# Performance work log

Measured on AMD Instinct MI355X. Metric: run time of the kernel, lower is better.

## Reference

```python
import jax, jax.numpy as jnp
import numpy as np

NUM_HEADS = 12
QUERY_SCALE = 0.125  # hard-coded 1/sqrt(64) in the original module


def setup_inputs() -> dict:
    key = jax.random.key(0)
    ks = jax.random.split(key, 5)
    S, B, H = 1024, 8, 768
    return {
        "hidden_states": jax.random.normal(ks[0], (S, B, H), dtype=jnp.float32),
        "in_proj_weight": jax.random.normal(ks[1], (3 * H, H), dtype=jnp.float32) * 0.02,
        "in_proj_bias": jax.random.normal(ks[2], (3 * H,), dtype=jnp.float32) * 0.02,
        "out_proj_weight": jax.random.normal(ks[3], (H, H), dtype=jnp.float32) * 0.02,
        "out_proj_bias": jax.random.normal(ks[4], (H,), dtype=jnp.float32) * 0.02,
    }


def reference(hidden_states, in_proj_weight, in_proj_bias, out_proj_weight, out_proj_bias):
    S, B, H = hidden_states.shape
    h = NUM_HEADS
    d = H // h

    # fused QKV in-projection: (S, B, 3H)
    mixed = hidden_states @ in_proj_weight.T + in_proj_bias
    q, k, v = jnp.split(mixed, 3, axis=-1)
    q = q * QUERY_SCALE

    def to_heads(x):  # (S, B, H) -> (B*h, S, d)
        return x.reshape(S, B * h, d).transpose(1, 0, 2)

    q, k, v = to_heads(q), to_heads(k), to_heads(v)

    scores = jnp.einsum("nsd,ntd->nst", q, k)          # (B*h, S, S)
    probs = jax.nn.softmax(scores, axis=-1)            # dropout is identity in eval
    ctx = jnp.einsum("nst,ntd->nsd", probs, v)         # (B*h, S, d)

    ctx = ctx.transpose(1, 0, 2).reshape(S, B, H)      # back to (S, B, H)
    return ctx @ out_proj_weight.T + out_proj_bias
```

## Files before the change

### kernel.cpp

```cpp
#include <hip/hip_runtime.h>

#define NH 12

typedef __bf16 bf16x8 __attribute__((ext_vector_type(8)));
typedef __bf16 bf16x4 __attribute__((ext_vector_type(4)));
typedef float f32x4 __attribute__((ext_vector_type(4)));

typedef const __attribute__((address_space(1))) void* gas_ptr;
typedef __attribute__((address_space(3))) void* las_ptr;

__device__ __forceinline__ void gload_lds16(const __bf16* g, __bf16* l) {
    __builtin_amdgcn_global_load_lds((gas_ptr)g, (las_ptr)l, 16, 0, 0);
}

#define QSCALE 0.18033688011112042f

__global__ void convert_kernel(const float* __restrict__ hs,
                               const float* __restrict__ w1,
                               const float* __restrict__ w2,
                               __bf16* __restrict__ xh,
                               __bf16* __restrict__ wq,
                               __bf16* __restrict__ wo) {
    const long long C0 = 786432;
    const long long C1 = 221184;
    const long long C2 = 73728;
    long long i = (long long)blockIdx.x * blockDim.x + threadIdx.x;
    const long long stride = (long long)gridDim.x * blockDim.x;
    for (; i < C0 + C1 + C2; i += stride) {
        const float* src; __bf16* dst; long long j;
        if (i < C0)           { src = hs; dst = xh; j = i; }
        else if (i < C0 + C1) { src = w1; dst = wq; j = i - C0; }
        else                  { src = w2; dst = wo; j = i - C0 - C1; }
        f32x4 v0 = *(const f32x4*)(src + j * 8);
        f32x4 v1 = *(const f32x4*)(src + j * 8 + 4);
        bf16x8 o;
#pragma unroll
        for (int r = 0; r < 4; r++) { o[r] = (__bf16)v0[r]; o[4 + r] = (__bf16)v1[r]; }
        *(bf16x8*)(dst + j * 8) = o;
    }
}

template <int MODE, int BM>
__global__ __launch_bounds__(BM * 4) void gemm_nt(
    const __bf16* __restrict__ A, const __bf16* __restrict__ Bm,
    const float* __restrict__ bias,
    __bf16* __restrict__ qb, __bf16* __restrict__ kb, __bf16* __restrict__ vT,
    float* __restrict__ outf, int M, int N, int K, int NXB)
{
    constexpr int THREADS = BM * 4;
    constexpr int ASZ = BM * 64 * 2;
    constexpr int BSZ = 128 * 64 * 2;
    constexpr int BUNITS = 1024 / THREADS;
    constexpr int SMEMSZ = (MODE == 0) ? 66560 : (2 * ASZ + 2 * BSZ);
    __shared__ __align__(16) char SMEM[SMEMSZ];

    const int t = threadIdx.x;
    const int lane = t & 63;
    const int w = t >> 6;
    const int wr = w >> 2, wc = w & 3;
    const int fr = lane & 15, g4 = lane >> 4;

    const int cpx = gridDim.x >> 3;
    const int orig = blockIdx.x;
    const int swz = (orig & 7) * cpx + (orig >> 3);
    const int bx = swz % NXB, by = swz / NXB;
    const int m0 = by * BM, n0 = bx * 128;

    f32x4 acc[4][2];
    const f32x4 z4 = {0.f, 0.f, 0.f, 0.f};
#pragma unroll
    for (int i = 0; i < 4; i++)
#pragma unroll
        for (int j = 0; j < 2; j++) acc[i][j] = z4;

    const int kSteps = K >> 6;

    auto As_ = [&](int b) { return (__bf16*)(SMEM + b * ASZ); };
    auto Bs_ = [&](int b) { return (__bf16*)(SMEM + 2 * ASZ + b * BSZ); };

    auto stage = [&](int tk, int b) {
#pragma unroll
        for (int u = 0; u < 2; u++) {
            const int c = u * THREADS + t;
            const int row = c >> 3;
            const int cb = ((c & 7) ^ (row & 7)) * 8;
            gload_lds16(A + (size_t)(m0 + row) * K + tk * 64 + cb, As_(b) + c * 8);
        }
#pragma unroll
        for (int u = 0; u < BUNITS; u++) {
            const int c = u * THREADS + t;
            const int row = c >> 3;
            const int cb = ((c & 7) ^ (row & 7)) * 8;
            gload_lds16(Bm + (size_t)(n0 + row) * K + tk * 64 + cb, Bs_(b) + c * 8);
        }
    };

    auto compute = [&](int cur) {
#pragma unroll
        for (int h = 0; h < 2; h++) {
            bf16x8 af[4], bfr[2];
#pragma unroll
            for (int i = 0; i < 4; i++) {
                const int r = wr * 64 + i * 16 + fr;
                af[i] = *(const bf16x8*)&As_(cur)[r * 64 + (((h * 4 + g4) ^ (r & 7)) * 8)];
            }
#pragma unroll
            for (int j = 0; j < 2; j++) {
                const int r = wc * 32 + j * 16 + fr;
                bfr[j] = *(const bf16x8*)&Bs_(cur)[r * 64 + (((h * 4 + g4) ^ (r & 7)) * 8)];
            }
            __builtin_amdgcn_s_setprio(1);
#pragma unroll
            for (int i = 0; i < 4; i++)
#pragma unroll
                for (int j = 0; j < 2; j++)
                    acc[i][j] = __builtin_amdgcn_mfma_f32_16x16x32_bf16(af[i], bfr[j], acc[i][j], 0, 0, 0);
            __builtin_amdgcn_s_setprio(0);
        }
    };

    stage(0, 0);
    __syncthreads();
    int cur = 0;
    for (int ks = 0; ks < kSteps; ks++) {
        if (ks < kSteps - 1) stage(ks + 1, cur ^ 1);
        compute(cur);
        __syncthreads();
        cur ^= 1;
    }

    if constexpr (MODE == 1) {
#pragma unroll
        for (int j = 0; j < 2; j++) {
            const int gc = n0 + wc * 32 + j * 16 + fr;
            const float bv = bias[gc];
#pragma unroll
            for (int i = 0; i < 4; i++)
#pragma unroll
                for (int r = 0; r < 4; r++) {
                    const int gr = m0 + wr * 64 + i * 16 + g4 * 4 + r;
                    outf[(size_t)gr * N + gc] = acc[i][j][r] + bv;
                }
        }
    } else {
        const int which = (n0 >= 1536) ? 2 : (n0 >= 768 ? 1 : 0);
        if (which < 2) {
#pragma unroll
            for (int j = 0; j < 2; j++) {
                const int gc = n0 + wc * 32 + j * 16 + fr;
                const float bv = bias[gc];
                const int jj = gc - which * 768;
                const int head = jj >> 6, dim = jj & 63;
#pragma unroll
                for (int i = 0; i < 4; i++)
#pragma unroll
                    for (int r = 0; r < 4; r++) {
                        const int gr = m0 + wr * 64 + i * 16 + g4 * 4 + r;
                        const int s = gr >> 3, b = gr & 7;
                        const size_t n = (size_t)(b * NH + head);
                        const float val = acc[i][j][r] + bv;
                        if (which == 0) qb[(n * 1024 + s) * 64 + dim] = (__bf16)(val * QSCALE);
                        else            kb[(n * 1024 + s) * 64 + dim] = (__bf16)val;
                    }
            }
        } else {
            float* Cw = (float*)SMEM;
#pragma unroll
            for (int j = 0; j < 2; j++) {
                const int col = wc * 32 + j * 16 + fr;
                const float bv = bias[n0 + col];
#pragma unroll
                for (int i = 0; i < 4; i++)
#pragma unroll
                    for (int r = 0; r < 4; r++) {
                        const int l = wr * 64 + i * 16 + g4 * 4 + r;
                        Cw[l * 130 + col] = acc[i][j][r] + bv;
                    }
            }
            __syncthreads();
            const int hbase = (n0 - 1536) >> 6;
            const int s0 = m0 >> 3;
#pragma unroll
            for (int u = 0; u < 2; u++) {
                const int c = u * THREADS + t;
                const int b = c >> 7;
                const int hd = (c >> 6) & 1;
                const int dim = c & 63;
                const size_t n = (size_t)(b * NH + hbase + hd);
                __bf16* dst = vT + (n * 64 + dim) * 1024 + s0;
                bf16x8 o0, o1;
#pragma unroll
                for (int sl = 0; sl < 8; sl++)
                    o0[sl] = (__bf16)Cw[(sl * 8 + b) * 130 + hd * 64 + dim];
#pragma unroll
                for (int sl = 0; sl < 8; sl++)
                    o1[sl] = (__bf16)Cw[((sl + 8) * 8 + b) * 130 + hd * 64 + dim];
                *(bf16x8*)dst = o0;
                *(bf16x8*)(dst + 8) = o1;
            }
        }
    }
}

__global__ __launch_bounds__(512) void attn_kernel(
    const __bf16* __restrict__ qb, const __bf16* __restrict__ kb,
    const __bf16* __restrict__ vT, __bf16* __restrict__ ctx)
{
    __shared__ __bf16 Kl[2][64 * 64];
    __shared__ __bf16 Vl[2][64 * 64];
    __shared__ __bf16 Pl[8][16 * 64];
    const int t = threadIdx.x, lane = t & 63, w = t >> 6;

    const int orig = blockIdx.x;
    const int swz = (orig & 7) * 96 + (orig >> 3);
    const int n = swz >> 3;
    const int q0 = (swz & 7) * 128;
    const int fr = lane & 15, g4 = lane >> 4;
    const int fx = fr & 7;

    const __bf16* qptr = qb + ((size_t)n * 1024 + q0 + w * 16 + fr) * 64 + g4 * 8;
    const bf16x8 qf0 = *(const bf16x8*)qptr;
    const bf16x8 qf1 = *(const bf16x8*)(qptr + 32);

    float mval = -1e30f, lval = 0.f;
    const f32x4 z4 = {0.f, 0.f, 0.f, 0.f};
    f32x4 o[4] = {z4, z4, z4, z4};

    const int srow = t >> 3;
    const int scb  = (t & 7) ^ (srow & 7);
    const __bf16* kbase = kb + (size_t)n * 65536;
    const __bf16* vbase = vT + (size_t)n * 65536;

    gload_lds16(kbase + (size_t)srow * 64 + scb * 8,   &Kl[0][t * 8]);
    gload_lds16(vbase + (size_t)srow * 1024 + scb * 8, &Vl[0][t * 8]);
    __syncthreads();

    int cur = 0;
    for (int kc = 0; kc < 16; kc++) {
        if (kc < 15) {
            const int t0 = (kc + 1) * 64;
            gload_lds16(kbase + (size_t)(t0 + srow) * 64 + scb * 8,  &Kl[cur ^ 1][t * 8]);
            gload_lds16(vbase + (size_t)srow * 1024 + t0 + scb * 8,  &Vl[cur ^ 1][t * 8]);
        }

        f32x4 sc[4];
        __builtin_amdgcn_s_setprio(1);
#pragma unroll
        for (int tt = 0; tt < 4; tt++) {
            const int row = (tt * 16 + fr) * 64;
            bf16x8 kf0 = *(const bf16x8*)&Kl[cur][row + ((g4 ^ fx) * 8)];
            bf16x8 kf1 = *(const bf16x8*)&Kl[cur][row + (((4 + g4) ^ fx) * 8)];
            f32x4 s = __builtin_amdgcn_mfma_f32_16x16x32_bf16(kf0, qf0, z4, 0, 0, 0);
            s = __builtin_amdgcn_mfma_f32_16x16x32_bf16(kf1, qf1, s, 0, 0, 0);
            sc[tt] = s;
        }
        __builtin_amdgcn_s_setprio(0);

        float a[16];
#pragma unroll
        for (int tt = 0; tt < 4; tt++)
#pragma unroll
            for (int r = 0; r < 4; r++) a[tt * 4 + r] = sc[tt][r];

        float m8[8];
#pragma unroll
        for (int i = 0; i < 8; i++) m8[i] = fmaxf(a[i], a[i + 8]);
        float m4a = fmaxf(m8[0], m8[4]), m4b = fmaxf(m8[1], m8[5]);
        float m4c = fmaxf(m8[2], m8[6]), m4d = fmaxf(m8[3], m8[7]);
        float pmax = fmaxf(fmaxf(m4a, m4b), fmaxf(m4c, m4d));
        pmax = fmaxf(pmax, __shfl_xor(pmax, 16));
        pmax = fmaxf(pmax, __shfl_xor(pmax, 32));

        if (pmax > mval + 8.0f) {
            const float sf = __builtin_amdgcn_exp2f(mval - pmax);
            lval *= sf;
#pragma unroll
            for (int dt = 0; dt < 4; dt++) o[dt] *= sf;
            mval = pmax;
        }

        float p[16];
#pragma unroll
        for (int i = 0; i < 16; i++) p[i] = __builtin_amdgcn_exp2f(a[i] - mval);
        float s8[8];
#pragma unroll
        for (int i = 0; i < 8; i++) s8[i] = p[i] + p[i + 8];
        float s4a = s8[0] + s8[4], s4b = s8[1] + s8[5];
        float s4c = s8[2] + s8[6], s4d = s8[3] + s8[7];
        float psum = (s4a + s4b) + (s4c + s4d);
        psum += __shfl_xor(psum, 16);
        psum += __shfl_xor(psum, 32);
        lval += psum;

#pragma unroll
        for (int tt = 0; tt < 4; tt++) {
            bf16x4 pk;
            pk[0] = (__bf16)p[tt * 4 + 0];
            pk[1] = (__bf16)p[tt * 4 + 1];
            pk[2] = (__bf16)p[tt * 4 + 2];
            pk[3] = (__bf16)p[tt * 4 + 3];
            const int blk = (2 * tt + (g4 >> 1)) ^ fx;
            *(bf16x4*)&Pl[w][fr * 64 + blk * 8 + (g4 & 1) * 4] = pk;
        }

        __builtin_amdgcn_s_setprio(1);
#pragma unroll
        for (int ks = 0; ks < 2; ks++) {
            bf16x8 pa = *(const bf16x8*)&Pl[w][fr * 64 + (((4 * ks + g4) ^ fx) * 8)];
#pragma unroll
            for (int dt = 0; dt < 4; dt++) {
                bf16x8 vf = *(const bf16x8*)&Vl[cur][(dt * 16 + fr) * 64 + (((4 * ks + g4) ^ fx) * 8)];
                o[dt] = __builtin_amdgcn_mfma_f32_16x16x32_bf16(vf, pa, o[dt], 0, 0, 0);
            }
        }
        __builtin_amdgcn_s_setprio(0);

        if (kc < 15) __syncthreads();
        cur ^= 1;
    }

    const int b = n / NH, head = n % NH;
    const float rl = 1.0f / lval;
    const int srw = q0 + w * 16 + fr;
    __bf16* cbase = ctx + ((size_t)srw * 8 + b) * 768 + head * 64;
#pragma unroll
    for (int dt = 0; dt < 4; dt++) {
        bf16x4 ov;
#pragma unroll
        for (int r = 0; r < 4; r++) ov[r] = (__bf16)(o[dt][r] * rl);
        *(bf16x4*)&cbase[dt * 16 + g4 * 4] = ov;
    }
}

extern "C" void kernel_launch(void* const* d_in, const int* in_sizes, int n_in,
                              void* d_out, int out_size, void* d_ws, size_t ws_size,
                              hipStream_t stream) {
    const float* hs = (const float*)d_in[0];
    const float* w1 = (const float*)d_in[1];
    const float* b1 = (const float*)d_in[2];
    const float* w2 = (const float*)d_in[3];
    const float* b2 = (const float*)d_in[4];
    float* out = (float*)d_out;

    char* ws = (char*)d_ws;
    __bf16* qb  = (__bf16*)(ws);
    __bf16* kb  = (__bf16*)(ws + 12582912);
    __bf16* vT  = (__bf16*)(ws + 25165824);
    __bf16* Xh  = (__bf16*)(ws + 37748736);
    __bf16* Wq  = (__bf16*)(ws + 50331648);
    __bf16* Wo  = (__bf16*)(ws + 53870592);
    __bf16* Ctx = Xh;

    convert_kernel<<<2048, 256, 0, stream>>>(hs, w1, w2, Xh, Wq, Wo);
    gemm_nt<0, 128><<<1152, 512, 0, stream>>>(Xh, Wq, b1, qb, kb, vT, nullptr, 8192, 2304, 768, 18);
    attn_kernel<<<768, 512, 0, stream>>>(qb, kb, vT, Ctx);
    gemm_nt<1, 64><<<768, 256, 0, stream>>>(Ctx, Wo, b2, nullptr, nullptr, nullptr, out, 8192, 768, 768, 6);
}
```

Baseline: 116.9 us.

## Fuse hidden-state bf16 conversion into QKV GEMM and read V directly from global

The QKV GEMM now loads fp32 hidden states into registers, converts them to bf16 and writes them to LDS after compute, instead of relying on a separate conversion pass that wrote a bf16 copy of X. The convert kernel now only handles the weights. Separately, the attention kernel drops the V LDS double buffer and loads V fragments straight from global memory into registers on each iteration. This removes a full write-then-read round trip of X and frees LDS, but it makes the A-operand path synchronous register loads instead of async global-to-LDS loads, and V reads now go uncached through LDS with a strided access pattern.

```diff
diff --git a/kernel.cpp b/kernel.cpp
--- a/kernel.cpp
+++ b/kernel.cpp
@@ -15,34 +15,30 @@
 
 #define QSCALE 0.18033688011112042f
 
-__global__ void convert_kernel(const float* __restrict__ hs,
-                               const float* __restrict__ w1,
-                               const float* __restrict__ w2,
-                               __bf16* __restrict__ xh,
-                               __bf16* __restrict__ wq,
-                               __bf16* __restrict__ wo) {
-    const long long C0 = 786432;
-    const long long C1 = 221184;
-    const long long C2 = 73728;
-    long long i = (long long)blockIdx.x * blockDim.x + threadIdx.x;
-    const long long stride = (long long)gridDim.x * blockDim.x;
-    for (; i < C0 + C1 + C2; i += stride) {
-        const float* src; __bf16* dst; long long j;
-        if (i < C0)           { src = hs; dst = xh; j = i; }
-        else if (i < C0 + C1) { src = w1; dst = wq; j = i - C0; }
-        else                  { src = w2; dst = wo; j = i - C0 - C1; }
-        f32x4 v0 = *(const f32x4*)(src + j * 8);
-        f32x4 v1 = *(const f32x4*)(src + j * 8 + 4);
+__global__ void convert_w(const float* __restrict__ w1,
+                          const float* __restrict__ w2,
+                          __bf16* __restrict__ wq,
+                          __bf16* __restrict__ wo) {
+    const int C1 = 221184;
+    const int C2 = 73728;
+    int i = blockIdx.x * blockDim.x + threadIdx.x;
+    const int stride = gridDim.x * blockDim.x;
+    for (; i < C1 + C2; i += stride) {
+        const float* src; __bf16* dst; int j;
+        if (i < C1) { src = w1; dst = wq; j = i; }
+        else        { src = w2; dst = wo; j = i - C1; }
+        f32x4 v0 = *(const f32x4*)(src + (size_t)j * 8);
+        f32x4 v1 = *(const f32x4*)(src + (size_t)j * 8 + 4);
         bf16x8 o;
 #pragma unroll
         for (int r = 0; r < 4; r++) { o[r] = (__bf16)v0[r]; o[4 + r] = (__bf16)v1[r]; }
-        *(bf16x8*)(dst + j * 8) = o;
+        *(bf16x8*)(dst + (size_t)j * 8) = o;
     }
 }
 
 template <int MODE, int BM>
 __global__ __launch_bounds__(BM * 4) void gemm_nt(
-    const __bf16* __restrict__ A, const __bf16* __restrict__ Bm,
+    const void* __restrict__ Av, const __bf16* __restrict__ Bm,
     const float* __restrict__ bias,
     __bf16* __restrict__ qb, __bf16* __restrict__ kb, __bf16* __restrict__ vT,
     float* __restrict__ outf, int M, int N, int K, int NXB)
@@ -78,14 +74,42 @@
     auto As_ = [&](int b) { return (__bf16*)(SMEM + b * ASZ); };
     auto Bs_ = [&](int b) { return (__bf16*)(SMEM + 2 * ASZ + b * BSZ); };
 
-    auto stage = [&](int tk, int b) {
+    int rowA[2], cbA[2], cA[2];
+#pragma unroll
+    for (int u = 0; u < 2; u++) {
+        const int c = u * THREADS + t;
+        rowA[u] = c >> 3;
+        cbA[u] = ((c & 7) ^ ((c >> 3) & 7)) * 8;
+        cA[u] = c;
+    }
+
+    const float*  Af = (const float*)Av;
+    const __bf16* Ab = (const __bf16*)Av;
+
+    f32x4 ar[2][2];
+    auto aload = [&](int tk) {
 #pragma unroll
         for (int u = 0; u < 2; u++) {
-            const int c = u * THREADS + t;
-            const int row = c >> 3;
-            const int cb = ((c & 7) ^ (row & 7)) * 8;
-            gload_lds16(A + (size_t)(m0 + row) * K + tk * 64 + cb, As_(b) + c * 8);
-        }
+            const float* p = Af + (size_t)(m0 + rowA[u]) * K + tk * 64 + cbA[u];
+            ar[u][0] = *(const f32x4*)p;
+            ar[u][1] = *(const f32x4*)(p + 4);
+        }
+    };
+    auto awrite = [&](int b) {
+#pragma unroll
+        for (int u = 0; u < 2; u++) {
+            bf16x8 o;
+#pragma unroll
+            for (int r = 0; r < 4; r++) { o[r] = (__bf16)ar[u][0][r]; o[4 + r] = (__bf16)ar[u][1][r]; }
+            *(bf16x8*)(As_(b) + cA[u] * 8) = o;
+        }
+    };
+    auto astage = [&](int tk, int b) {
+#pragma unroll
+        for (int u = 0; u < 2; u++)
+            gload_lds16(Ab + (size_t)(m0 + rowA[u]) * K + tk * 64 + cbA[u], As_(b) + cA[u] * 8);
+    };
+    auto bstage = [&](int tk, int b) {
 #pragma unroll
         for (int u = 0; u < BUNITS; u++) {
             const int c = u * THREADS + t;
@@ -119,12 +143,18 @@
         }
     };
 
-    stage(0, 0);
+    if constexpr (MODE == 0) { aload(0); awrite(0); } else { astage(0, 0); }
+    bstage(0, 0);
     __syncthreads();
     int cur = 0;
     for (int ks = 0; ks < kSteps; ks++) {
-        if (ks < kSteps - 1) stage(ks + 1, cur ^ 1);
+        if (ks < kSteps - 1) {
+            if constexpr (MODE == 0) aload(ks + 1);
+            else                     astage(ks + 1, cur ^ 1);
+            bstage(ks + 1, cur ^ 1);
+        }
         compute(cur);
+        if constexpr (MODE == 0) { if (ks < kSteps - 1) awrite(cur ^ 1); }
         __syncthreads();
         cur ^= 1;
     }
@@ -207,7 +237,6 @@
     const __bf16* __restrict__ vT, __bf16* __restrict__ ctx)
 {
     __shared__ __bf16 Kl[2][64 * 64];
-    __shared__ __bf16 Vl[2][64 * 64];
     __shared__ __bf16 Pl[8][16 * 64];
     const int t = threadIdx.x, lane = t & 63, w = t >> 6;
 
@@ -231,17 +260,20 @@
     const __bf16* kbase = kb + (size_t)n * 65536;
     const __bf16* vbase = vT + (size_t)n * 65536;
 
-    gload_lds16(kbase + (size_t)srow * 64 + scb * 8,   &Kl[0][t * 8]);
-    gload_lds16(vbase + (size_t)srow * 1024 + scb * 8, &Vl[0][t * 8]);
+    gload_lds16(kbase + (size_t)srow * 64 + scb * 8, &Kl[0][t * 8]);
     __syncthreads();
 
     int cur = 0;
     for (int kc = 0; kc < 16; kc++) {
-        if (kc < 15) {
-            const int t0 = (kc + 1) * 64;
-            gload_lds16(kbase + (size_t)(t0 + srow) * 64 + scb * 8,  &Kl[cur ^ 1][t * 8]);
-            gload_lds16(vbase + (size_t)srow * 1024 + t0 + scb * 8,  &Vl[cur ^ 1][t * 8]);
-        }
+        if (kc < 15)
+            gload_lds16(kbase + (size_t)((kc + 1) * 64 + srow) * 64 + scb * 8, &Kl[cur ^ 1][t * 8]);
+
+        bf16x8 vf[2][4];
+#pragma unroll
+        for (int ks = 0; ks < 2; ks++)
+#pragma unroll
+            for (int dt = 0; dt < 4; dt++)
+                vf[ks][dt] = *(const bf16x8*)(vbase + (size_t)(dt * 16 + fr) * 1024 + kc * 64 + ks * 32 + g4 * 8);
 
         f32x4 sc[4];
         __builtin_amdgcn_s_setprio(1);
@@ -308,10 +340,8 @@
         for (int ks = 0; ks < 2; ks++) {
             bf16x8 pa = *(const bf16x8*)&Pl[w][fr * 64 + (((4 * ks + g4) ^ fx) * 8)];
 #pragma unroll
-            for (int dt = 0; dt < 4; dt++) {
-                bf16x8 vf = *(const bf16x8*)&Vl[cur][(dt * 16 + fr) * 64 + (((4 * ks + g4) ^ fx) * 8)];
-                o[dt] = __builtin_amdgcn_mfma_f32_16x16x32_bf16(vf, pa, o[dt], 0, 0, 0);
-            }
+            for (int dt = 0; dt < 4; dt++)
+                o[dt] = __builtin_amdgcn_mfma_f32_16x16x32_bf16(vf[ks][dt], pa, o[dt], 0, 0, 0);
         }
         __builtin_amdgcn_s_setprio(0);
 
@@ -346,13 +376,12 @@
     __bf16* qb  = (__bf16*)(ws);
     __bf16* kb  = (__bf16*)(ws + 12582912);
     __bf16* vT  = (__bf16*)(ws + 25165824);
-    __bf16* Xh  = (__bf16*)(ws + 37748736);
+    __bf16* Ctx = (__bf16*)(ws + 37748736);
     __bf16* Wq  = (__bf16*)(ws + 50331648);
     __bf16* Wo  = (__bf16*)(ws + 53870592);
-    __bf16* Ctx = Xh;
-
-    convert_kernel<<<2048, 256, 0, stream>>>(hs, w1, w2, Xh, Wq, Wo);
-    gemm_nt<0, 128><<<1152, 512, 0, stream>>>(Xh, Wq, b1, qb, kb, vT, nullptr, 8192, 2304, 768, 18);
+
+    convert_w<<<512, 256, 0, stream>>>(w1, w2, Wq, Wo);
+    gemm_nt<0, 128><<<1152, 512, 0, stream>>>(hs, Wq, b1, qb, kb, vT, nullptr, 8192, 2304, 768, 18);
     attn_kernel<<<768, 512, 0, stream>>>(qb, kb, vT, Ctx);
     gemm_nt<1, 64><<<768, 256, 0, stream>>>(Ctx, Wo, b2, nullptr, nullptr, nullptr, out, 8192, 768, 768, 6);
 }
```

Result: slower. 177.0 us (+51.4%).
